# Performance work log

Hardware: AMD Instinct MI355X
Metric: run time of the kernel (lower is better)

Reference implementation:

```python
import jax, jax.numpy as jnp
import numpy as np

NEG_SLOPE = 0.2


def gatv2_layer(x, edge_index, Wl, Wr, att, bias):
    """PyG GATv2Conv (share_weights=False, concat=True, negative_slope=0.2).
    x: [N, F]; Wl/Wr: [F, H*C]; att: [H, C]; bias: [H*C]. Returns [N, H*C]."""
    N = x.shape[0]
    H, C = att.shape
    src, dst = edge_index[0], edge_index[1]
    xl = (x @ Wl).reshape(N, H, C)  # source transform
    xr = (x @ Wr).reshape(N, H, C)  # target transform
    # per-edge attention logits
    e = jax.nn.leaky_relu(xl[src] + xr[dst], NEG_SLOPE)          # [E, H, C]
    logits = jnp.einsum('ehc,hc->eh', e, att)                     # [E, H]
    # segment softmax over incoming edges of each destination node
    m = jax.ops.segment_max(logits, dst, num_segments=N)          # [N, H]
    m = jnp.where(jnp.isfinite(m), m, 0.0)                        # empty segments
    ex = jnp.exp(logits - m[dst])                                 # [E, H]
    denom = jax.ops.segment_sum(ex, dst, num_segments=N)          # [N, H]
    alpha = ex / (denom[dst] + 1e-16)                             # [E, H]
    msg = xl[src] * alpha[..., None]                              # [E, H, C]
    out = jax.ops.segment_sum(msg, dst, num_segments=N)           # [N, H, C]
    return out.reshape(N, H * C) + bias


def setup_inputs() -> dict:
    key = jax.random.key(0)
    ks = jax.random.split(key, 10)
    N, E, F, H, C, OUT = 50000, 800000, 256, 8, 32, 64
    s = 0.05
    return {
        'x': jax.random.normal(ks[0], (N, F), dtype=jnp.float32),
        'edge_index': jax.random.randint(ks[1], (2, E), 0, N, dtype=jnp.int64),
        'Wl1': jax.random.normal(ks[2], (F, H * C), dtype=jnp.float32) * s,
        'Wr1': jax.random.normal(ks[3], (F, H * C), dtype=jnp.float32) * s,
        'att1': jax.random.normal(ks[4], (H, C), dtype=jnp.float32) * s,
        'b1': jax.random.normal(ks[5], (H * C,), dtype=jnp.float32) * s,
        'Wl2': jax.random.normal(ks[6], (H * C, OUT), dtype=jnp.float32) * s,
        'Wr2': jax.random.normal(ks[7], (H * C, OUT), dtype=jnp.float32) * s,
        'att2': jax.random.normal(ks[8], (1, OUT), dtype=jnp.float32) * s,
        'b2': jax.random.normal(ks[9], (OUT,), dtype=jnp.float32) * s,
    }


def reference(x, edge_index, Wl1, Wr1, att1, b1, Wl2, Wr2, att2, b2):
    h = gatv2_layer(x, edge_index, Wl1, Wr1, att1, b1)
    h = jax.nn.relu(h)
    h = gatv2_layer(h, edge_index, Wl2, Wr2, att2, b2)
    return (h, jax.nn.log_softmax(h, axis=1))
```

## Files before the change

### kernel.cpp

```cpp
#include <hip/hip_runtime.h>
#include <hip/hip_bf16.h>
#include <math.h>

#define NEG_SLOPE 0.2f

typedef __attribute__((ext_vector_type(8))) short short8;
typedef __attribute__((ext_vector_type(4))) float floatx4;

__device__ inline ushort f2b(float f) {
    __hip_bfloat16 b = __float2bfloat16(f);
    return *(ushort*)&b;
}
__device__ inline float b2f(ushort u) {
    union { unsigned int i; float f; } c;
    c.i = ((unsigned int)u) << 16;
    return c.f;
}

template<int BM, int BN, typename AT>
__global__ __launch_bounds__(256) void gemm_bf16(const AT* __restrict__ A,
                                                 const ushort* __restrict__ Bt,
                                                 ushort* __restrict__ C,
                                                 int M, int N, int K)
{
    constexpr int SA = 40;
    __shared__ ushort As[BM * SA];
    __shared__ ushort Bs[BN * SA];
    const int tid = threadIdx.x;
    const int w = tid >> 6, lane = tid & 63;
    const int mw = (w & 1) * 64;
    const int nw = (w >> 1) * 64;
    const int m0 = blockIdx.y * BM;
    const int n0 = blockIdx.x * BN;
    const int lm = lane & 15;
    const int kg = lane >> 4;

    floatx4 acc[4][4];
#pragma unroll
    for (int i = 0; i < 4; ++i)
#pragma unroll
        for (int j = 0; j < 4; ++j) acc[i][j] = (floatx4)0.f;

    for (int k0 = 0; k0 < K; k0 += 32) {
#pragma unroll
        for (int it = 0; it < BM / 64; ++it) {
            int idx = it * 256 + tid;
            int row = idx >> 2, kc = idx & 3;
            int grow = m0 + row;
            if (grow >= M) grow = M - 1;
            if constexpr (sizeof(AT) == 4) {
                float4 f0 = *(const float4*)&A[(size_t)grow * K + k0 + kc * 8];
                float4 f1 = *(const float4*)&A[(size_t)grow * K + k0 + kc * 8 + 4];
                ushort* d = &As[row * SA + kc * 8];
                d[0] = f2b(f0.x); d[1] = f2b(f0.y); d[2] = f2b(f0.z); d[3] = f2b(f0.w);
                d[4] = f2b(f1.x); d[5] = f2b(f1.y); d[6] = f2b(f1.z); d[7] = f2b(f1.w);
            } else {
                short8 v = *(const short8*)&A[(size_t)grow * K + k0 + kc * 8];
                *(short8*)&As[row * SA + kc * 8] = v;
            }
        }
#pragma unroll
        for (int it = 0; it < BN / 64; ++it) {
            int idx = it * 256 + tid;
            int row = idx >> 2, kc = idx & 3;
            short8 v = *(const short8*)&Bt[(size_t)(n0 + row) * K + k0 + kc * 8];
            *(short8*)&Bs[row * SA + kc * 8] = v;
        }
        __syncthreads();
        short8 a[4], b[4];
#pragma unroll
        for (int i = 0; i < 4; ++i)
            a[i] = *(const short8*)&As[(mw + i * 16 + lm) * SA + kg * 8];
#pragma unroll
        for (int j = 0; j < 4; ++j)
            b[j] = *(const short8*)&Bs[(nw + j * 16 + lm) * SA + kg * 8];
#pragma unroll
        for (int i = 0; i < 4; ++i)
#pragma unroll
            for (int j = 0; j < 4; ++j)
                acc[i][j] = __builtin_amdgcn_mfma_f32_16x16x32_bf16(a[i], b[j], acc[i][j], 0, 0, 0);
        __syncthreads();
    }

#pragma unroll
    for (int i = 0; i < 4; ++i) {
        int rbase = m0 + mw + i * 16 + (lane >> 4) * 4;
#pragma unroll
        for (int j = 0; j < 4; ++j) {
            int col = n0 + nw + j * 16 + lm;
#pragma unroll
            for (int r = 0; r < 4; ++r) {
                int row = rbase + r;
                if (row < M) C[(size_t)row * N + col] = f2b(acc[i][j][r]);
            }
        }
    }
}

__global__ void k_tcast(const float* __restrict__ W, ushort* __restrict__ Wt, int K, int N)
{
    int i = blockIdx.x * blockDim.x + threadIdx.x;
    if (i < K * N) {
        int k = i / N, n = i % N;
        Wt[(size_t)n * K + k] = f2b(W[i]);
    }
}

__global__ void k_count(const int* __restrict__ dst, int E, int* __restrict__ counts)
{
    int i = blockIdx.x * blockDim.x + threadIdx.x;
    if (i < E) atomicAdd(&counts[dst[i]], 1);
}

__global__ void k_chunksum(const int* __restrict__ counts, int N, int* __restrict__ chunk)
{
    __shared__ int sm[256];
    const int t = threadIdx.x;
    const int base = blockIdx.x * 1024;
    int s = 0;
    for (int i = t; i < 1024; i += 256) {
        int idx = base + i;
        s += (idx < N) ? counts[idx] : 0;
    }
    sm[t] = s;
    __syncthreads();
    for (int off = 128; off; off >>= 1) {
        if (t < off) sm[t] += sm[t + off];
        __syncthreads();
    }
    if (t == 0) chunk[blockIdx.x] = sm[0];
}

__global__ void k_scanchunk(int* __restrict__ chunk, int nchunks)
{
    if (blockIdx.x == 0 && threadIdx.x == 0) {
        int run = 0;
        for (int i = 0; i < nchunks; ++i) {
            int c = chunk[i];
            chunk[i] = run;
            run += c;
        }
        chunk[nchunks] = run;
    }
}

__global__ void k_scanwrite(const int* __restrict__ counts, int N,
                            const int* __restrict__ chunk,
                            int* __restrict__ offsets, int* __restrict__ cursor)
{
    __shared__ int sm[256];
    const int t = threadIdx.x;
    const int base = blockIdx.x * 1024 + t * 4;
    int v[4];
    int s = 0;
#pragma unroll
    for (int i = 0; i < 4; ++i) {
        v[i] = (base + i < N) ? counts[base + i] : 0;
        s += v[i];
    }
    sm[t] = s;
    __syncthreads();
    for (int off = 1; off < 256; off <<= 1) {
        int y = (t >= off) ? sm[t - off] : 0;
        __syncthreads();
        sm[t] += y;
        __syncthreads();
    }
    int run = chunk[blockIdx.x] + sm[t] - s;
#pragma unroll
    for (int i = 0; i < 4; ++i) {
        if (base + i < N) {
            offsets[base + i] = run;
            cursor[base + i] = run;
        }
        run += v[i];
    }
    if (blockIdx.x == 0 && t == 0) offsets[N] = chunk[gridDim.x];
}

__global__ void k_fill(const int* __restrict__ src, const int* __restrict__ dst,
                       int E, int* __restrict__ cursor, int* __restrict__ csr_src)
{
    int i = blockIdx.x * blockDim.x + threadIdx.x;
    if (i < E) {
        int d = dst[i];
        int pos = atomicAdd(&cursor[d], 1);
        csr_src[pos] = src[i];
    }
}

__global__ __launch_bounds__(256) void agg1(const ushort* __restrict__ xlr,
                                            const float* __restrict__ att,
                                            const float* __restrict__ bias,
                                            const int* __restrict__ offsets,
                                            const int* __restrict__ csr_src,
                                            ushort* __restrict__ h1, int N)
{
    const int wave = blockIdx.x * 4 + (threadIdx.x >> 6);
    const int lane = threadIdx.x & 63;
    if (wave >= N) return;
    const int n = wave;
    const int g = lane >> 5;
    const int sl = lane & 31;
    const int elem = (sl >> 2) * 32 + (sl & 3) * 8;

    float attv[8], xrv[8];
    {
        short8 xr8 = *(const short8*)&xlr[(size_t)n * 512 + 256 + elem];
#pragma unroll
        for (int j = 0; j < 8; ++j) {
            attv[j] = att[elem + j];
            xrv[j] = b2f((ushort)xr8[j]);
        }
    }
    float m = -1e30f, l = 0.f;
    float acc[8] = {0.f, 0.f, 0.f, 0.f, 0.f, 0.f, 0.f, 0.f};

    const int beg = offsets[n], end = offsets[n + 1];
    short8 xv;
    {
        int k = beg + g;
        if (k < end) xv = *(const short8*)&xlr[(size_t)csr_src[k] * 512 + elem];
    }
    for (int kb = beg; kb < end; kb += 2) {
        const int kk = kb + g;
        short8 cur = xv;
        {
            int kn = kk + 2;
            if (kn < end) xv = *(const short8*)&xlr[(size_t)csr_src[kn] * 512 + elem];
        }
        if (kk < end) {
            float xlv[8];
#pragma unroll
            for (int j = 0; j < 8; ++j) xlv[j] = b2f((ushort)cur[j]);
            float u = 0.f;
#pragma unroll
            for (int j = 0; j < 8; ++j) {
                float t = xlv[j] + xrv[j];
                t = fmaxf(t, NEG_SLOPE * t);
                u = fmaf(t, attv[j], u);
            }
            u += __shfl_xor(u, 1);
            u += __shfl_xor(u, 2);
            float e = __expf(-fabsf(u - m));
            bool keep = (m >= u);
            float sc = keep ? 1.f : e;
            float p  = keep ? e : 1.f;
            m = fmaxf(m, u);
#pragma unroll
            for (int j = 0; j < 8; ++j) acc[j] = fmaf(acc[j], sc, p * xlv[j]);
            l = fmaf(l, sc, p);
        }
    }
    {
        float mo = __shfl_xor(m, 32);
        float lo = __shfl_xor(l, 32);
        float nm = fmaxf(m, mo);
        float ea = __expf(m - nm);
        float eb = __expf(mo - nm);
#pragma unroll
        for (int j = 0; j < 8; ++j) {
            float ao = __shfl_xor(acc[j], 32);
            acc[j] = acc[j] * ea + ao * eb;
        }
        l = l * ea + lo * eb;
    }
    if (g == 0) {
        float rl = 1.f / (l + 1e-16f);
        short8 o;
#pragma unroll
        for (int j = 0; j < 8; ++j) {
            float v = fmaf(acc[j], rl, bias[elem + j]);
            o[j] = (short)f2b(fmaxf(v, 0.f));
        }
        *(short8*)&h1[(size_t)n * 256 + elem] = o;
    }
}

__global__ __launch_bounds__(256) void agg2(const ushort* __restrict__ xlr,
                                            const float* __restrict__ att,
                                            const float* __restrict__ bias,
                                            const int* __restrict__ offsets,
                                            const int* __restrict__ csr_src,
                                            float* __restrict__ out, int N)
{
    const int wave = blockIdx.x * 4 + (threadIdx.x >> 6);
    const int lane = threadIdx.x & 63;
    if (wave >= N) return;
    const int n = wave;
    const int g = lane >> 4;
    const int c0 = (lane & 15) * 4;

    const float4 attv = *(const float4*)&att[c0];
    ushort4 xr4 = *(const ushort4*)&xlr[(size_t)n * 128 + 64 + c0];
    float xrv[4] = {b2f(xr4.x), b2f(xr4.y), b2f(xr4.z), b2f(xr4.w)};

    float m = -1e30f, l = 0.f;
    float acc[4] = {0.f, 0.f, 0.f, 0.f};

    const int beg = offsets[n], end = offsets[n + 1];
    for (int kb = beg; kb < end; kb += 4) {
        int k = kb + g;
        if (k < end) {
            int s = csr_src[k];
            ushort4 xv = *(const ushort4*)&xlr[(size_t)s * 128 + c0];
            float xlv[4] = {b2f(xv.x), b2f(xv.y), b2f(xv.z), b2f(xv.w)};
            float u = 0.f;
#pragma unroll
            for (int j = 0; j < 4; ++j) {
                float t = xlv[j] + xrv[j];
                t = fmaxf(t, NEG_SLOPE * t);
                u = fmaf(t, ((const float*)&attv)[j], u);
            }
            u += __shfl_xor(u, 1);
            u += __shfl_xor(u, 2);
            u += __shfl_xor(u, 4);
            u += __shfl_xor(u, 8);
            float e = __expf(-fabsf(u - m));
            bool keep = (m >= u);
            float sc = keep ? 1.f : e;
            float p  = keep ? e : 1.f;
            m = fmaxf(m, u);
#pragma unroll
            for (int j = 0; j < 4; ++j) acc[j] = fmaf(acc[j], sc, p * xlv[j]);
            l = fmaf(l, sc, p);
        }
    }
#pragma unroll
    for (int off = 16; off <= 32; off <<= 1) {
        float mo = __shfl_xor(m, off);
        float lo = __shfl_xor(l, off);
        float ao[4];
#pragma unroll
        for (int j = 0; j < 4; ++j) ao[j] = __shfl_xor(acc[j], off);
        float nm = fmaxf(m, mo);
        float sa = __expf(m - nm);
        float sb = __expf(mo - nm);
#pragma unroll
        for (int j = 0; j < 4; ++j) acc[j] = acc[j] * sa + ao[j] * sb;
        l = l * sa + lo * sb;
        m = nm;
    }
    float rl = 1.f / (l + 1e-16f);
    const float4 bv = *(const float4*)&bias[c0];
    float h[4];
#pragma unroll
    for (int j = 0; j < 4; ++j) h[j] = acc[j] * rl + ((const float*)&bv)[j];

    float mx = fmaxf(fmaxf(h[0], h[1]), fmaxf(h[2], h[3]));
    mx = fmaxf(mx, __shfl_xor(mx, 1));
    mx = fmaxf(mx, __shfl_xor(mx, 2));
    mx = fmaxf(mx, __shfl_xor(mx, 4));
    mx = fmaxf(mx, __shfl_xor(mx, 8));
    float ssum = __expf(h[0] - mx) + __expf(h[1] - mx) + __expf(h[2] - mx) + __expf(h[3] - mx);
    ssum += __shfl_xor(ssum, 1);
    ssum += __shfl_xor(ssum, 2);
    ssum += __shfl_xor(ssum, 4);
    ssum += __shfl_xor(ssum, 8);
    float lg = __logf(ssum);
    if (g == 0) {
        float4 o1 = make_float4(h[0], h[1], h[2], h[3]);
        *(float4*)&out[(size_t)n * 64 + c0] = o1;
        float4 o2 = make_float4(h[0] - mx - lg, h[1] - mx - lg, h[2] - mx - lg, h[3] - mx - lg);
        *(float4*)&out[(size_t)(N + n) * 64 + c0] = o2;
    }
}

extern "C" void kernel_launch(void* const* d_in, const int* in_sizes, int n_in,
                              void* d_out, int out_size, void* d_ws, size_t ws_size,
                              hipStream_t stream)
{
    const float* x    = (const float*)d_in[0];
    const int*   ei   = (const int*)d_in[1];
    const float* Wl1  = (const float*)d_in[2];
    const float* Wr1  = (const float*)d_in[3];
    const float* att1 = (const float*)d_in[4];
    const float* b1   = (const float*)d_in[5];
    const float* Wl2  = (const float*)d_in[6];
    const float* Wr2  = (const float*)d_in[7];
    const float* att2 = (const float*)d_in[8];
    const float* b2   = (const float*)d_in[9];
    float* out = (float*)d_out;

    const int F = 256;
    const int E = in_sizes[1] / 2;
    const int N = in_sizes[0] / F;

    const int* e_src = ei;
    const int* e_dst = ei + E;

    ushort* wlr1t = (ushort*)d_ws;
    ushort* wlr2t = wlr1t + 512 * 256;
    ushort* xlr1  = wlr2t + 128 * 256;
    ushort* h1b   = xlr1 + (size_t)N * 512;
    ushort* xlr2  = h1b + (size_t)N * 256;
    int* offsets  = (int*)(xlr2 + (size_t)N * 128);
    int* cursor   = offsets + (N + 1);
    int* counts   = cursor + (N + 1);
    int* chunkoff = counts + N;
    int* csr_src  = chunkoff + 66;

    const int nchunks = (N + 1023) / 1024;

    k_tcast<<<(256 * 256 + 255) / 256, 256, 0, stream>>>(Wl1, wlr1t, 256, 256);
    k_tcast<<<(256 * 256 + 255) / 256, 256, 0, stream>>>(Wr1, wlr1t + 256 * 256, 256, 256);
    k_tcast<<<(256 * 64 + 255) / 256, 256, 0, stream>>>(Wl2, wlr2t, 256, 64);
    k_tcast<<<(256 * 64 + 255) / 256, 256, 0, stream>>>(Wr2, wlr2t + 64 * 256, 256, 64);

    hipMemsetAsync(counts, 0, (size_t)N * sizeof(int), stream);
    k_count<<<(E + 255) / 256, 256, 0, stream>>>(e_dst, E, counts);
    k_chunksum<<<nchunks, 256, 0, stream>>>(counts, N, chunkoff);
    k_scanchunk<<<1, 64, 0, stream>>>(chunkoff, nchunks);
    k_scanwrite<<<nchunks, 256, 0, stream>>>(counts, N, chunkoff, offsets, cursor);
    k_fill<<<(E + 255) / 256, 256, 0, stream>>>(e_src, e_dst, E, cursor, csr_src);

    gemm_bf16<128, 128, float><<<dim3(4, (N + 127) / 128), 256, 0, stream>>>(x, wlr1t, xlr1, N, 512, F);
    agg1<<<(N + 3) / 4, 256, 0, stream>>>(xlr1, att1, b1, offsets, csr_src, h1b, N);

    gemm_bf16<128, 128, ushort><<<dim3(1, (N + 127) / 128), 256, 0, stream>>>(h1b, wlr2t, xlr2, N, 128, 256);
    agg2<<<(N + 3) / 4, 256, 0, stream>>>(xlr2, att2, b2, offsets, csr_src, out, N);
}
```

Before: 374.9 us.

## Fuse weight prep with edge counting, packed-float aggregation, smaller second GEMM tiles

Merges the four weight transpose-cast kernels and the edge-count kernel into a single launch, and reorders the first GEMM before the CSR scan. Rewrites both aggregation kernels to use packed two-wide float math with unconditional clamped prefetch. Adds software prefetch to agg2. Changes the second GEMM to 128x64 tiles with two column blocks, giving more blocks for the narrow output. These steps aim to cut launch overhead and raise memory-level parallelism, at the cost of redundant clamped loads on the last edges.

```diff
diff --git a/kernel.cpp b/kernel.cpp
--- a/kernel.cpp
+++ b/kernel.cpp
@@ -6,6 +6,7 @@
 
 typedef __attribute__((ext_vector_type(8))) short short8;
 typedef __attribute__((ext_vector_type(4))) float floatx4;
+typedef __attribute__((ext_vector_type(2))) float floatx2;
 
 __device__ inline ushort f2b(float f) {
     __hip_bfloat16 b = __float2bfloat16(f);
@@ -15,6 +16,13 @@
     union { unsigned int i; float f; } c;
     c.i = ((unsigned int)u) << 16;
     return c.f;
+}
+__device__ inline floatx2 bf2x2(unsigned int d) {
+    union { unsigned int i; float f; } lo, hi;
+    lo.i = d << 16;
+    hi.i = d & 0xffff0000u;
+    floatx2 r = {lo.f, hi.f};
+    return r;
 }
 
 template<int BM, int BN, typename AT>
@@ -24,22 +32,26 @@
                                                  int M, int N, int K)
 {
     constexpr int SA = 40;
+    constexpr int WTM = (BN == 64) ? 32 : 64;
+    constexpr int WM  = BM / WTM;
+    constexpr int IT  = WTM / 16;
+    constexpr int JT  = 4;
     __shared__ ushort As[BM * SA];
     __shared__ ushort Bs[BN * SA];
     const int tid = threadIdx.x;
     const int w = tid >> 6, lane = tid & 63;
-    const int mw = (w & 1) * 64;
-    const int nw = (w >> 1) * 64;
+    const int mw = (w % WM) * WTM;
+    const int nw = (w / WM) * 64;
     const int m0 = blockIdx.y * BM;
     const int n0 = blockIdx.x * BN;
     const int lm = lane & 15;
     const int kg = lane >> 4;
 
-    floatx4 acc[4][4];
-#pragma unroll
-    for (int i = 0; i < 4; ++i)
-#pragma unroll
-        for (int j = 0; j < 4; ++j) acc[i][j] = (floatx4)0.f;
+    floatx4 acc[IT][JT];
+#pragma unroll
+    for (int i = 0; i < IT; ++i)
+#pragma unroll
+        for (int j = 0; j < JT; ++j) acc[i][j] = (floatx4)0.f;
 
     for (int k0 = 0; k0 < K; k0 += 32) {
 #pragma unroll
@@ -67,26 +79,26 @@
             *(short8*)&Bs[row * SA + kc * 8] = v;
         }
         __syncthreads();
-        short8 a[4], b[4];
-#pragma unroll
-        for (int i = 0; i < 4; ++i)
+        short8 a[IT], b[JT];
+#pragma unroll
+        for (int i = 0; i < IT; ++i)
             a[i] = *(const short8*)&As[(mw + i * 16 + lm) * SA + kg * 8];
 #pragma unroll
-        for (int j = 0; j < 4; ++j)
+        for (int j = 0; j < JT; ++j)
             b[j] = *(const short8*)&Bs[(nw + j * 16 + lm) * SA + kg * 8];
 #pragma unroll
-        for (int i = 0; i < 4; ++i)
-#pragma unroll
-            for (int j = 0; j < 4; ++j)
+        for (int i = 0; i < IT; ++i)
+#pragma unroll
+            for (int j = 0; j < JT; ++j)
                 acc[i][j] = __builtin_amdgcn_mfma_f32_16x16x32_bf16(a[i], b[j], acc[i][j], 0, 0, 0);
         __syncthreads();
     }
 
 #pragma unroll
-    for (int i = 0; i < 4; ++i) {
+    for (int i = 0; i < IT; ++i) {
         int rbase = m0 + mw + i * 16 + (lane >> 4) * 4;
 #pragma unroll
-        for (int j = 0; j < 4; ++j) {
+        for (int j = 0; j < JT; ++j) {
             int col = n0 + nw + j * 16 + lm;
 #pragma unroll
             for (int r = 0; r < 4; ++r) {
@@ -97,19 +109,35 @@
     }
 }
 
-__global__ void k_tcast(const float* __restrict__ W, ushort* __restrict__ Wt, int K, int N)
-{
-    int i = blockIdx.x * blockDim.x + threadIdx.x;
-    if (i < K * N) {
-        int k = i / N, n = i % N;
-        Wt[(size_t)n * K + k] = f2b(W[i]);
-    }
-}
-
-__global__ void k_count(const int* __restrict__ dst, int E, int* __restrict__ counts)
-{
-    int i = blockIdx.x * blockDim.x + threadIdx.x;
-    if (i < E) atomicAdd(&counts[dst[i]], 1);
+__global__ void k_prep(const float* __restrict__ Wl1, const float* __restrict__ Wr1,
+                       const float* __restrict__ Wl2, const float* __restrict__ Wr2,
+                       ushort* __restrict__ wlr1t, ushort* __restrict__ wlr2t,
+                       const int* __restrict__ dst, int E, int* __restrict__ counts)
+{
+    const int b = blockIdx.x;
+    const int t = threadIdx.x;
+    if (b < 640) {
+        int i = b * 256 + t;
+        if (i < 65536) {
+            int k = i >> 8, n = i & 255;
+            wlr1t[n * 256 + k] = f2b(Wl1[i]);
+        } else if (i < 131072) {
+            int j = i - 65536;
+            int k = j >> 8, n = j & 255;
+            wlr1t[65536 + n * 256 + k] = f2b(Wr1[j]);
+        } else if (i < 147456) {
+            int j = i - 131072;
+            int k = j >> 6, n = j & 63;
+            wlr2t[n * 256 + k] = f2b(Wl2[j]);
+        } else {
+            int j = i - 147456;
+            int k = j >> 6, n = j & 63;
+            wlr2t[16384 + n * 256 + k] = f2b(Wr2[j]);
+        }
+    } else {
+        int i = (b - 640) * 256 + t;
+        if (i < E) atomicAdd(&counts[dst[i]], 1);
+    }
 }
 
 __global__ void k_chunksum(const int* __restrict__ counts, int N, int* __restrict__ chunk)
@@ -204,52 +232,58 @@
     const int sl = lane & 31;
     const int elem = (sl >> 2) * 32 + (sl & 3) * 8;
 
-    float attv[8], xrv[8];
+    floatx2 attv2[4], xrv2[4];
     {
-        short8 xr8 = *(const short8*)&xlr[(size_t)n * 512 + 256 + elem];
-#pragma unroll
-        for (int j = 0; j < 8; ++j) {
-            attv[j] = att[elem + j];
-            xrv[j] = b2f((ushort)xr8[j]);
+        uint4 xr8 = *(const uint4*)&xlr[(size_t)n * 512 + 256 + elem];
+        unsigned int xw[4] = {xr8.x, xr8.y, xr8.z, xr8.w};
+#pragma unroll
+        for (int i = 0; i < 4; ++i) {
+            attv2[i] = *(const floatx2*)&att[elem + 2 * i];
+            xrv2[i] = bf2x2(xw[i]);
         }
     }
     float m = -1e30f, l = 0.f;
-    float acc[8] = {0.f, 0.f, 0.f, 0.f, 0.f, 0.f, 0.f, 0.f};
+    floatx2 acc2[4] = {(floatx2)0.f, (floatx2)0.f, (floatx2)0.f, (floatx2)0.f};
 
     const int beg = offsets[n], end = offsets[n + 1];
-    short8 xv;
-    {
-        int k = beg + g;
-        if (k < end) xv = *(const short8*)&xlr[(size_t)csr_src[k] * 512 + elem];
-    }
-    for (int kb = beg; kb < end; kb += 2) {
-        const int kk = kb + g;
-        short8 cur = xv;
+    if (beg < end) {
+        uint4 xv;
         {
-            int kn = kk + 2;
-            if (kn < end) xv = *(const short8*)&xlr[(size_t)csr_src[kn] * 512 + elem];
-        }
-        if (kk < end) {
-            float xlv[8];
-#pragma unroll
-            for (int j = 0; j < 8; ++j) xlv[j] = b2f((ushort)cur[j]);
-            float u = 0.f;
-#pragma unroll
-            for (int j = 0; j < 8; ++j) {
-                float t = xlv[j] + xrv[j];
-                t = fmaxf(t, NEG_SLOPE * t);
-                u = fmaf(t, attv[j], u);
-            }
-            u += __shfl_xor(u, 1);
-            u += __shfl_xor(u, 2);
-            float e = __expf(-fabsf(u - m));
-            bool keep = (m >= u);
-            float sc = keep ? 1.f : e;
-            float p  = keep ? e : 1.f;
-            m = fmaxf(m, u);
-#pragma unroll
-            for (int j = 0; j < 8; ++j) acc[j] = fmaf(acc[j], sc, p * xlv[j]);
-            l = fmaf(l, sc, p);
+            int k0 = beg + g;
+            int ks = (k0 < end) ? k0 : end - 1;
+            xv = *(const uint4*)&xlr[(size_t)csr_src[ks] * 512 + elem];
+        }
+        for (int kb = beg; kb < end; kb += 2) {
+            const int kk = kb + g;
+            uint4 cur = xv;
+            {
+                int kn = kk + 2;
+                int ks = (kn < end) ? kn : end - 1;
+                xv = *(const uint4*)&xlr[(size_t)csr_src[ks] * 512 + elem];
+            }
+            if (kk < end) {
+                unsigned int cw[4] = {cur.x, cur.y, cur.z, cur.w};
+                floatx2 xl2[4];
+                floatx2 u2 = (floatx2)0.f;
+#pragma unroll
+                for (int i = 0; i < 4; ++i) {
+                    xl2[i] = bf2x2(cw[i]);
+                    floatx2 t = xl2[i] + xrv2[i];
+                    t = __builtin_elementwise_max(t, t * NEG_SLOPE);
+                    u2 += t * attv2[i];
+                }
+                float u = u2.x + u2.y;
+                u += __shfl_xor(u, 1);
+                u += __shfl_xor(u, 2);
+                float e = __expf(-fabsf(u - m));
+                bool kp = (m >= u);
+                float sc = kp ? 1.f : e;
+                float p  = kp ? e : 1.f;
+                m = fmaxf(m, u);
+#pragma unroll
+                for (int i = 0; i < 4; ++i) acc2[i] = acc2[i] * sc + xl2[i] * p;
+                l = fmaf(l, sc, p);
+            }
         }
     }
     {
@@ -259,9 +293,9 @@
         float ea = __expf(m - nm);
         float eb = __expf(mo - nm);
 #pragma unroll
-        for (int j = 0; j < 8; ++j) {
-            float ao = __shfl_xor(acc[j], 32);
-            acc[j] = acc[j] * ea + ao * eb;
+        for (int i = 0; i < 4; ++i) {
+            floatx2 ao = {__shfl_xor(acc2[i].x, 32), __shfl_xor(acc2[i].y, 32)};
+            acc2[i] = acc2[i] * ea + ao * eb;
         }
         l = l * ea + lo * eb;
     }
@@ -269,9 +303,11 @@
         float rl = 1.f / (l + 1e-16f);
         short8 o;
 #pragma unroll
-        for (int j = 0; j < 8; ++j) {
-            float v = fmaf(acc[j], rl, bias[elem + j]);
-            o[j] = (short)f2b(fmaxf(v, 0.f));
+        for (int i = 0; i < 4; ++i) {
+            float v0 = fmaf(acc2[i].x, rl, bias[elem + 2 * i]);
+            float v1 = fmaf(acc2[i].y, rl, bias[elem + 2 * i + 1]);
+            o[2 * i]     = (short)f2b(fmaxf(v0, 0.f));
+            o[2 * i + 1] = (short)f2b(fmaxf(v1, 0.f));
         }
         *(short8*)&h1[(size_t)n * 256 + elem] = o;
     }
@@ -291,61 +327,81 @@
     const int g = lane >> 4;
     const int c0 = (lane & 15) * 4;
 
-    const float4 attv = *(const float4*)&att[c0];
-    ushort4 xr4 = *(const ushort4*)&xlr[(size_t)n * 128 + 64 + c0];
-    float xrv[4] = {b2f(xr4.x), b2f(xr4.y), b2f(xr4.z), b2f(xr4.w)};
-
+    floatx2 attv2[2], xrv2[2];
+    {
+        uint2 xr4 = *(const uint2*)&xlr[(size_t)n * 128 + 64 + c0];
+        attv2[0] = *(const floatx2*)&att[c0];
+        attv2[1] = *(const floatx2*)&att[c0 + 2];
+        xrv2[0] = bf2x2(xr4.x);
+        xrv2[1] = bf2x2(xr4.y);
+    }
     float m = -1e30f, l = 0.f;
-    float acc[4] = {0.f, 0.f, 0.f, 0.f};
+    floatx2 acc2[2] = {(floatx2)0.f, (floatx2)0.f};
 
     const int beg = offsets[n], end = offsets[n + 1];
-    for (int kb = beg; kb < end; kb += 4) {
-        int k = kb + g;
-        if (k < end) {
-            int s = csr_src[k];
-            ushort4 xv = *(const ushort4*)&xlr[(size_t)s * 128 + c0];
-            float xlv[4] = {b2f(xv.x), b2f(xv.y), b2f(xv.z), b2f(xv.w)};
-            float u = 0.f;
-#pragma unroll
-            for (int j = 0; j < 4; ++j) {
-                float t = xlv[j] + xrv[j];
-                t = fmaxf(t, NEG_SLOPE * t);
-                u = fmaf(t, ((const float*)&attv)[j], u);
-            }
-            u += __shfl_xor(u, 1);
-            u += __shfl_xor(u, 2);
-            u += __shfl_xor(u, 4);
-            u += __shfl_xor(u, 8);
-            float e = __expf(-fabsf(u - m));
-            bool keep = (m >= u);
-            float sc = keep ? 1.f : e;
-            float p  = keep ? e : 1.f;
-            m = fmaxf(m, u);
-#pragma unroll
-            for (int j = 0; j < 4; ++j) acc[j] = fmaf(acc[j], sc, p * xlv[j]);
-            l = fmaf(l, sc, p);
+    if (beg < end) {
+        uint2 xv;
+        {
+            int k0 = beg + g;
+            int ks = (k0 < end) ? k0 : end - 1;
+            xv = *(const uint2*)&xlr[(size_t)csr_src[ks] * 128 + c0];
+        }
+        for (int kb = beg; kb < end; kb += 4) {
+            const int kk = kb + g;
+            uint2 cur = xv;
+            {
+                int kn = kk + 4;
+                int ks = (kn < end) ? kn : end - 1;
+                xv = *(const uint2*)&xlr[(size_t)csr_src[ks] * 128 + c0];
+            }
+            if (kk < end) {
+                floatx2 xl2[2];
+                xl2[0] = bf2x2(cur.x);
+                xl2[1] = bf2x2(cur.y);
+                floatx2 u2 = (floatx2)0.f;
+#pragma unroll
+                for (int i = 0; i < 2; ++i) {
+                    floatx2 t = xl2[i] + xrv2[i];
+                    t = __builtin_elementwise_max(t, t * NEG_SLOPE);
+                    u2 += t * attv2[i];
+                }
+                float u = u2.x + u2.y;
+                u += __shfl_xor(u, 1);
+                u += __shfl_xor(u, 2);
+                u += __shfl_xor(u, 4);
+                u += __shfl_xor(u, 8);
+                float e = __expf(-fabsf(u - m));
+                bool kp = (m >= u);
+                float sc = kp ? 1.f : e;
+                float p  = kp ? e : 1.f;
+                m = fmaxf(m, u);
+#pragma unroll
+                for (int i = 0; i < 2; ++i) acc2[i] = acc2[i] * sc + xl2[i] * p;
+                l = fmaf(l, sc, p);
+            }
         }
     }
 #pragma unroll
     for (int off = 16; off <= 32; off <<= 1) {
         float mo = __shfl_xor(m, off);
         float lo = __shfl_xor(l, off);
-        float ao[4];
-#pragma unroll
-        for (int j = 0; j < 4; ++j) ao[j] = __shfl_xor(acc[j], off);
         float nm = fmaxf(m, mo);
         float sa = __expf(m - nm);
         float sb = __expf(mo - nm);
 #pragma unroll
-        for (int j = 0; j < 4; ++j) acc[j] = acc[j] * sa + ao[j] * sb;
+        for (int i = 0; i < 2; ++i) {
+            floatx2 ao = {__shfl_xor(acc2[i].x, off), __shfl_xor(acc2[i].y, off)};
+            acc2[i] = acc2[i] * sa + ao * sb;
+        }
         l = l * sa + lo * sb;
         m = nm;
     }
     float rl = 1.f / (l + 1e-16f);
-    const float4 bv = *(const float4*)&bias[c0];
     float h[4];
-#pragma unroll
-    for (int j = 0; j < 4; ++j) h[j] = acc[j] * rl + ((const float*)&bv)[j];
+    h[0] = acc2[0].x * rl + bias[c0];
+    h[1] = acc2[0].y * rl + bias[c0 + 1];
+    h[2] = acc2[1].x * rl + bias[c0 + 2];
+    h[3] = acc2[1].y * rl + bias[c0 + 3];
 
     float mx = fmaxf(fmaxf(h[0], h[1]), fmaxf(h[2], h[3]));
     mx = fmaxf(mx, __shfl_xor(mx, 1));
@@ -402,21 +458,19 @@
 
     const int nchunks = (N + 1023) / 1024;
 
-    k_tcast<<<(256 * 256 + 255) / 256, 256, 0, stream>>>(Wl1, wlr1t, 256, 256);
-    k_tcast<<<(256 * 256 + 255) / 256, 256, 0, stream>>>(Wr1, wlr1t + 256 * 256, 256, 256);
-    k_tcast<<<(256 * 64 + 255) / 256, 256, 0, stream>>>(Wl2, wlr2t, 256, 64);
-    k_tcast<<<(256 * 64 + 255) / 256, 256, 0, stream>>>(Wr2, wlr2t + 64 * 256, 256, 64);
-
     hipMemsetAsync(counts, 0, (size_t)N * sizeof(int), stream);
-    k_count<<<(E + 255) / 256, 256, 0, stream>>>(e_dst, E, counts);
+    k_prep<<<640 + (E + 255) / 256, 256, 0, stream>>>(Wl1, Wr1, Wl2, Wr2,
+                                                      wlr1t, wlr2t, e_dst, E, counts);
+
+    gemm_bf16<128, 128, float><<<dim3(4, (N + 127) / 128), 256, 0, stream>>>(x, wlr1t, xlr1, N, 512, F);
+
     k_chunksum<<<nchunks, 256, 0, stream>>>(counts, N, chunkoff);
     k_scanchunk<<<1, 64, 0, stream>>>(chunkoff, nchunks);
     k_scanwrite<<<nchunks, 256, 0, stream>>>(counts, N, chunkoff, offsets, cursor);
     k_fill<<<(E + 255) / 256, 256, 0, stream>>>(e_src, e_dst, E, cursor, csr_src);
 
-    gemm_bf16<128, 128, float><<<dim3(4, (N + 127) / 128), 256, 0, stream>>>(x, wlr1t, xlr1, N, 512, F);
     agg1<<<(N + 3) / 4, 256, 0, stream>>>(xlr1, att1, b1, offsets, csr_src, h1b, N);
 
-    gemm_bf16<128, 128, ushort><<<dim3(1, (N + 127) / 128), 256, 0, stream>>>(h1b, wlr2t, xlr2, N, 128, 256);
+    gemm_bf16<128, 64, ushort><<<dim3(2, (N + 127) / 128), 256, 0, stream>>>(h1b, wlr2t, xlr2, N, 128, 256);
     agg2<<<(N + 3) / 4, 256, 0, stream>>>(xlr2, att2, b2, offsets, csr_src, out, N);
 }
```

After: 358.1 us. -4.5%, faster.
